# Kernel optimization log

Hardware: AMD Instinct MI355X
Metric: run time of the kernel (lower is better)

The kernel has to match this reference:

```python
import jax, jax.numpy as jnp
import numpy as np

N_NODES = 50000
N_EDGES = 1600000
HID = 128
REST = 96  # (hidden//4) x 1e vectors = 32*3
N_MP = 2


def _linear_init(key, fan_in, fan_out):
    return jax.random.normal(key, (fan_in, fan_out), dtype=jnp.float32) / np.sqrt(fan_in)


def setup_inputs() -> dict:
    key = jax.random.key(0)
    ks = jax.random.split(key, 16)
    h = jax.random.normal(ks[0], (N_NODES, HID + REST), dtype=jnp.float32)
    edge_index = jax.random.randint(ks[1], (2, N_EDGES), 0, N_NODES, dtype=jnp.int32)
    edge_len = jax.random.uniform(ks[2], (N_EDGES,), dtype=jnp.float32) * 5.0
    # ScalarMessagePassing MLPs: Linear(2*HID+1 -> HID), SiLU, Linear(HID -> HID), stacked per layer
    mp_w1 = jnp.stack([_linear_init(ks[3 + i], 2 * HID + 1, HID) for i in range(N_MP)])
    mp_b1 = jnp.zeros((N_MP, HID), dtype=jnp.float32)
    mp_w2 = jnp.stack([_linear_init(ks[5 + i], HID, HID) for i in range(N_MP)])
    mp_b2 = jnp.zeros((N_MP, HID), dtype=jnp.float32)
    # NodeUpdateMLP: Linear(HID -> HID), SiLU, Linear(HID -> HID)
    nu_w1 = _linear_init(ks[7], HID, HID)
    nu_b1 = jnp.zeros((HID,), dtype=jnp.float32)
    nu_w2 = _linear_init(ks[8], HID, HID)
    nu_b2 = jnp.zeros((HID,), dtype=jnp.float32)
    return dict(h=h, edge_index=edge_index, edge_len=edge_len,
                mp_w1=mp_w1, mp_b1=mp_b1, mp_w2=mp_w2, mp_b2=mp_b2,
                nu_w1=nu_w1, nu_b1=nu_b1, nu_w2=nu_w2, nu_b2=nu_b2)


def _scalar_mp(scalars, sender, receiver, edge_len, w1, b1, w2, b2):
    # gather -> MLP -> index_add scatter, residual on scalar channels
    msg_in = jnp.concatenate([scalars[sender], scalars[receiver], edge_len[:, None]], axis=-1)  # [E, 2H+1]
    msgs = jax.nn.silu(msg_in @ w1 + b1) @ w2 + b2  # [E, H]
    agg = jax.ops.segment_sum(msgs, receiver, num_segments=scalars.shape[0])  # [N, H]
    return scalars + agg


def reference(h, edge_index, edge_len, mp_w1, mp_b1, mp_w2, mp_b2, nu_w1, nu_b1, nu_w2, nu_b2):
    scalars, rest = h[..., :HID], h[..., HID:]
    sender, receiver = edge_index[0], edge_index[1]
    for i in range(N_MP):
        scalars = _scalar_mp(scalars, sender, receiver, edge_len,
                             mp_w1[i], mp_b1[i], mp_w2[i], mp_b2[i])
    # NodeUpdateMLP: scalars + MLP(scalars)
    scalars = scalars + (jax.nn.silu(scalars @ nu_w1 + nu_b1) @ nu_w2 + nu_b2)
    return jnp.concatenate([scalars, rest], axis=-1)
```

## Files before the change

kernel.cpp:

```cpp
#include <hip/hip_runtime.h>
#include <hip/hip_fp16.h>


#define NFEAT 224
#define RBITS 8
#define NB 196
#define CAP 10240

typedef _Float16 v8h __attribute__((ext_vector_type(8)));
typedef _Float16 v2h __attribute__((ext_vector_type(2)));
typedef float f32x4 __attribute__((ext_vector_type(4)));

#define MFMA16(a, b, c) __builtin_amdgcn_mfma_f32_16x16x32_f16(a, b, c, 0, 0, 0)

__device__ __forceinline__ float silu_f(float x) {
    float e = __expf(-x);
    return x * __builtin_amdgcn_rcpf(1.0f + e);
}

__global__ void k_prep(const float* __restrict__ mp_w1, const float* __restrict__ mp_w2,
                       const float* __restrict__ nu_w1, const float* __restrict__ nu_w2,
                       _Float16* __restrict__ Wp,
                       const float4* __restrict__ h4, float4* __restrict__ out4, int N) {
    if (blockIdx.x < 8) {
        const float* srcs[8] = {
            mp_w1, mp_w1 + 16384, mp_w2,
            mp_w1 + 32896, mp_w1 + 32896 + 16384, mp_w2 + 16384,
            nu_w1, nu_w2
        };
        const float* W = srcs[blockIdx.x];
        _Float16* dst = Wp + (size_t)blockIdx.x * 16384;
        for (int i = 0; i < 8; ++i) {
            int u = threadIdx.x + i * 256;
            int nt = u >> 8;
            int kt = (u >> 6) & 3;
            int lane = u & 63;
            int kb = kt * 32 + (lane >> 4) * 8;
            int n = nt * 16 + (lane & 15);
#pragma unroll
            for (int j = 0; j < 8; ++j)
                dst[(size_t)u * 8 + j] = (_Float16)W[(size_t)(kb + j) * 128 + n];
        }
    } else {
        int b = blockIdx.x - 8;
        int t = threadIdx.x;
        if (t < 240) {
            int r = b * 10 + t / 24;
            int c = t % 24;
            if (r < N) out4[(size_t)r * 56 + 32 + c] = h4[(size_t)r * 56 + 32 + c];
        }
    }
}

__global__ void cs_bucket(const int* __restrict__ recv, const int* __restrict__ sender,
                          const float* __restrict__ elen, int* __restrict__ cnt,
                          int* __restrict__ br, unsigned* __restrict__ bsl,
                          int E, int chunk) {
    __shared__ int lhist[256];
    __shared__ int lcur[256];
    int t = threadIdx.x;
    int start = blockIdx.x * chunk;
    int end = start + chunk; if (end > E) end = E;
    lhist[t] = 0;
    __syncthreads();
    for (int i = start + t; i < end; i += 256)
        atomicAdd(&lhist[recv[i] >> RBITS], 1);
    __syncthreads();
    if (t < NB) {
        int c = lhist[t];
        lcur[t] = t * CAP + (c ? atomicAdd(&cnt[t], c) : 0);
    }
    __syncthreads();
    for (int i = start + t; i < end; i += 256) {
        int r = recv[i];
        int pos = atomicAdd(&lcur[r >> RBITS], 1);
        br[pos] = r;
        bsl[pos] = (unsigned)sender[i] |
                   ((unsigned)__half_as_ushort(__float2half_rn(elen[i])) << 16);
    }
}

__global__ void cs_csr(const int* __restrict__ cnt, const int* __restrict__ br,
                       const unsigned* __restrict__ bsl,
                       int* __restrict__ deg, int* __restrict__ rowstart,
                       unsigned* __restrict__ epack, int N) {
    __shared__ int hist[256];
    __shared__ int sh[256];
    __shared__ int lcur[256];
    int t = threadIdx.x;
    int b = blockIdx.x;
    int r0 = b << RBITS;
    int e0 = b * CAP;
    int e1 = e0 + cnt[b];
    hist[t] = 0;
    __syncthreads();
    for (int i = e0 + t; i < e1; i += 256)
        atomicAdd(&hist[br[i] & 255], 1);
    __syncthreads();
    sh[t] = hist[t];
    __syncthreads();
    for (int off = 1; off < 256; off <<= 1) {
        int add = (t >= off) ? sh[t - off] : 0;
        __syncthreads();
        sh[t] += add;
        __syncthreads();
    }
    int excl = (t == 0) ? 0 : sh[t - 1];
    lcur[t] = e0 + excl;
    int r = r0 + t;
    if (r < N) { deg[r] = hist[t]; rowstart[r] = e0 + excl; }
    __syncthreads();
    for (int i = e0 + t; i < e1; i += 256) {
        int rr = br[i];
        int pos = atomicAdd(&lcur[rr & 255], 1);
        epack[pos] = bsl[i];
    }
}


#define MM_STAGE_A_F32(Aptr, ldA)                                           \
    _Pragma("unroll") for (int i = 0; i < 4; ++i) {                         \
        int u = threadIdx.x + i * 256;                                      \
        int r = u >> 4;                                                     \
        int g = u & 15;                                                     \
        int gr = blockIdx.x * 64 + r;                                       \
        float4 x0 = make_float4(0.f, 0.f, 0.f, 0.f);                        \
        float4 x1 = x0;                                                     \
        if (gr < M) {                                                       \
            const float* s_ = (Aptr) + (size_t)gr * (ldA) + g * 8;          \
            x0 = *(const float4*)s_;                                        \
            x1 = *(const float4*)(s_ + 4);                                  \
        }                                                                   \
        v8h hv;                                                             \
        hv[0] = (_Float16)x0.x; hv[1] = (_Float16)x0.y;                     \
        hv[2] = (_Float16)x0.z; hv[3] = (_Float16)x0.w;                     \
        hv[4] = (_Float16)x1.x; hv[5] = (_Float16)x1.y;                     \
        hv[6] = (_Float16)x1.z; hv[7] = (_Float16)x1.w;                     \
        Af[((r >> 4) * 4 + (g >> 2)) * 64 + (g & 3) * 16 + (r & 15)] = hv;  \
    }

#define MM_STAGE_A_F16(Aptr)                                                \
    _Pragma("unroll") for (int i = 0; i < 4; ++i) {                         \
        int u = threadIdx.x + i * 256;                                      \
        int r = u >> 4;                                                     \
        int g = u & 15;                                                     \
        int gr = blockIdx.x * 64 + r;                                       \
        float4 x = make_float4(0.f, 0.f, 0.f, 0.f);                         \
        if (gr < M) x = *(const float4*)((Aptr) + (size_t)gr * 128 + g * 8);\
        *(float4*)&Af[((r >> 4) * 4 + (g >> 2)) * 64 + (g & 3) * 16 + (r & 15)] = x; \
    }

#define MM_WAVE_PROLOG                                                      \
    __syncthreads();                                                        \
    const int wv = threadIdx.x >> 6;                                        \
    const int lane = threadIdx.x & 63;                                      \
    const int q_ = lane >> 4;                                               \
    const int c0_ = lane & 15;                                              \
    v8h a0 = Af[(wv * 4 + 0) * 64 + lane];                                  \
    v8h a1 = Af[(wv * 4 + 1) * 64 + lane];                                  \
    v8h a2 = Af[(wv * 4 + 2) * 64 + lane];                                  \
    v8h a3 = Af[(wv * 4 + 3) * 64 + lane];                                  \
    const int grb = blockIdx.x * 64 + wv * 16 + q_ * 4;

#define MM_RELOAD_A(SRC)                                                    \
    a0 = SRC[(wv * 4 + 0) * 64 + lane];                                     \
    a1 = SRC[(wv * 4 + 1) * 64 + lane];                                     \
    a2 = SRC[(wv * 4 + 2) * 64 + lane];                                     \
    a3 = SRC[(wv * 4 + 3) * 64 + lane];

#define MM_COMPUTE_B(WPTR, ...)                                             \
    {                                                                       \
        const v8h* Bp_ = (const v8h*)(WPTR) + lane;                         \
        _Pragma("unroll") for (int nt = 0; nt < 8; ++nt) {                  \
            v8h b0 = Bp_[nt * 256];                                         \
            v8h b1v = Bp_[nt * 256 + 64];                                   \
            v8h b2v = Bp_[nt * 256 + 128];                                  \
            v8h b3v = Bp_[nt * 256 + 192];                                  \
            f32x4 c = {0.f, 0.f, 0.f, 0.f};                                 \
            c = MFMA16(a0, b0, c);                                          \
            c = MFMA16(a1, b1v, c);                                         \
            c = MFMA16(a2, b2v, c);                                         \
            c = MFMA16(a3, b3v, c);                                         \
            const int col = nt * 16 + c0_;                                  \
            __VA_ARGS__                                                     \
        }                                                                   \
    }

#define MM_EXCHANGE_IDX                                                     \
    int kt = col >> 5;                                                      \
    int o = col & 31;                                                       \
    int qp = o >> 3;                                                        \
    int j = o & 7;                                                          \
    int base = ((wv * 4 + kt) * 64 + qp * 16 + q_ * 4) * 8 + j;

__launch_bounds__(256)
__global__ void k_mm_xsrb2(const float* __restrict__ A, int ldA,
                           const _Float16* __restrict__ Wp0, const float* __restrict__ b1,
                           _Float16* __restrict__ Xs, _Float16* __restrict__ Xrb, int M) {
    __shared__ v8h Af[1024];
    MM_STAGE_A_F32(A, ldA)
    MM_WAVE_PROLOG
    MM_COMPUTE_B(Wp0, {
        _Pragma("unroll") for (int i = 0; i < 4; ++i) {
            int gr = grb + i;
            if (gr < M) Xs[(size_t)gr * 128 + col] = (_Float16)c[i];
        }
    })
    MM_COMPUTE_B(Wp0 + 16384, {
        float bc = b1[col];
        _Pragma("unroll") for (int i = 0; i < 4; ++i) {
            int gr = grb + i;
            if (gr < M) Xrb[(size_t)gr * 128 + col] = (_Float16)(c[i] + bc);
        }
    })
}

__launch_bounds__(256)
__global__ void k_mm_accxsrb(const _Float16* __restrict__ P, const _Float16* __restrict__ Ww2,
                             const float* __restrict__ b2, const int* __restrict__ deg,
                             const float* __restrict__ Sin, int ldSin,
                             float* __restrict__ Sout,
                             const _Float16* __restrict__ Wp1, const float* __restrict__ b1,
                             _Float16* __restrict__ Xs, _Float16* __restrict__ Xrb, int M) {
    __shared__ v8h Af[1024];
    __shared__ v8h Af2[1024];
    MM_STAGE_A_F16(P)
    MM_WAVE_PROLOG
    _Float16* A2 = (_Float16*)Af2;
    MM_COMPUTE_B(Ww2, {
        float bc = b2[col];
        MM_EXCHANGE_IDX
        _Pragma("unroll") for (int i = 0; i < 4; ++i) {
            int gr = grb + i;
            float sv = 0.f;
            if (gr < M) {
                sv = Sin[(size_t)gr * ldSin + col] + c[i] + bc * (float)deg[gr];
                Sout[(size_t)gr * 128 + col] = sv;
            }
            A2[base + i * 8] = (_Float16)sv;
        }
    })
    __syncthreads();
    MM_RELOAD_A(Af2)
    MM_COMPUTE_B(Wp1, {
        _Pragma("unroll") for (int i = 0; i < 4; ++i) {
            int gr = grb + i;
            if (gr < M) Xs[(size_t)gr * 128 + col] = (_Float16)c[i];
        }
    })
    MM_COMPUTE_B(Wp1 + 16384, {
        float bc = b1[col];
        _Pragma("unroll") for (int i = 0; i < 4; ++i) {
            int gr = grb + i;
            if (gr < M) Xrb[(size_t)gr * 128 + col] = (_Float16)(c[i] + bc);
        }
    })
}

__launch_bounds__(256)
__global__ void k_mm_accnode(const _Float16* __restrict__ P, const _Float16* __restrict__ Ww2,
                             const float* __restrict__ b2, const int* __restrict__ deg,
                             const float* __restrict__ Sin,
                             const _Float16* __restrict__ Wn1, const float* __restrict__ nb1,
                             const _Float16* __restrict__ Wn2, const float* __restrict__ nb2,
                             float* __restrict__ out, int M) {
    __shared__ v8h Af[1024];
    __shared__ v8h Af2[1024];
    MM_STAGE_A_F16(P)
    MM_WAVE_PROLOG
    float s2v[8][4];
    _Float16* A2 = (_Float16*)Af2;
    MM_COMPUTE_B(Ww2, {
        float bc = b2[col];
        MM_EXCHANGE_IDX
        _Pragma("unroll") for (int i = 0; i < 4; ++i) {
            int gr = grb + i;
            float sv = 0.f;
            if (gr < M) sv = Sin[(size_t)gr * 128 + col] + c[i] + bc * (float)deg[gr];
            s2v[nt][i] = sv;
            A2[base + i * 8] = (_Float16)sv;
        }
    })
    __syncthreads();
    MM_RELOAD_A(Af2)
    _Float16* A3 = (_Float16*)Af;
    MM_COMPUTE_B(Wn1, {
        float bc = nb1[col];
        MM_EXCHANGE_IDX
        _Pragma("unroll") for (int i = 0; i < 4; ++i)
            A3[base + i * 8] = (_Float16)silu_f(c[i] + bc);
    })
    __syncthreads();
    MM_RELOAD_A(Af)
    MM_COMPUTE_B(Wn2, {
        float bc = nb2[col];
        _Pragma("unroll") for (int i = 0; i < 4; ++i) {
            int gr = grb + i;
            if (gr < M)
                out[(size_t)gr * NFEAT + col] = s2v[nt][i] + c[i] + bc;
        }
    })
}

__device__ __forceinline__ v2h silu2_pk(v2h pre) {
    const v2h h27 = {(_Float16)27.f, (_Float16)27.f};
    const v2h hp3 = {(_Float16)3.f, (_Float16)3.f};
    const v2h hn3 = {(_Float16)-3.f, (_Float16)-3.f};
    v2h h = pre * (_Float16)0.5f;
    v2h z = __builtin_elementwise_min(__builtin_elementwise_max(h, hn3), hp3);
    v2h z2 = z * z;
    v2h num = z * (z2 + h27);
    v2h den = z2 * (_Float16)9.f + h27;
    __half2 rd = h2rcp(__builtin_bit_cast(__half2, den));
    v2h u = num * __builtin_bit_cast(v2h, rd);
    return h * u + h;
}

__launch_bounds__(256)
__global__ void k_edge(const v2h* __restrict__ Xs, const v2h* __restrict__ Xrb,
                       const float* __restrict__ w1L, const unsigned* __restrict__ epack,
                       const int* __restrict__ rowstart, const int* __restrict__ deg,
                       v2h* __restrict__ P, int N) {
    int wid = (blockIdx.x * blockDim.x + threadIdx.x) >> 6;
    int lane = threadIdx.x & 63;
    if (wid >= N) return;
    int lo = __builtin_amdgcn_readfirstlane(rowstart[wid]);
    int dg = __builtin_amdgcn_readfirstlane(deg[wid]);
    const unsigned* ep = epack + lo;
    v2h xr = Xrb[(size_t)wid * 64 + lane];
    float2 wlf = *(const float2*)(w1L + lane * 2);
    v2h wl = {(_Float16)wlf.x, (_Float16)wlf.y};
    float ax = 0.f, ay = 0.f;
    int k = 0;
    unsigned pc[8];
    v2h xc[8];
    if (dg >= 8) {
#pragma unroll
        for (int u = 0; u < 8; ++u) pc[u] = ep[u];
#pragma unroll
        for (int u = 0; u < 8; ++u)
            xc[u] = Xs[(size_t)(pc[u] & 0xFFFFu) * 64 + lane];
    }
    for (; k + 16 <= dg; k += 8) {
        unsigned pn[8];
        v2h xn[8];
#pragma unroll
        for (int u = 0; u < 8; ++u) pn[u] = ep[k + 8 + u];
#pragma unroll
        for (int u = 0; u < 8; ++u)
            xn[u] = Xs[(size_t)(pn[u] & 0xFFFFu) * 64 + lane];
        v2h t2 = {(_Float16)0.f, (_Float16)0.f};
#pragma unroll
        for (int u = 0; u < 8; ++u) {
            _Float16 lv = __builtin_bit_cast(_Float16, (unsigned short)(pc[u] >> 16));
            v2h pre = xc[u] + xr + lv * wl;
            t2 = t2 + silu2_pk(pre);
        }
        ax += (float)t2[0]; ay += (float)t2[1];
#pragma unroll
        for (int u = 0; u < 8; ++u) { pc[u] = pn[u]; xc[u] = xn[u]; }
    }
    if (k + 8 <= dg) {
        v2h t2 = {(_Float16)0.f, (_Float16)0.f};
#pragma unroll
        for (int u = 0; u < 8; ++u) {
            _Float16 lv = __builtin_bit_cast(_Float16, (unsigned short)(pc[u] >> 16));
            v2h pre = xc[u] + xr + lv * wl;
            t2 = t2 + silu2_pk(pre);
        }
        ax += (float)t2[0]; ay += (float)t2[1];
        k += 8;
    }
    for (; k < dg; ++k) {
        unsigned p = ep[k];
        _Float16 lv = __builtin_bit_cast(_Float16, (unsigned short)(p >> 16));
        v2h x = Xs[(size_t)(p & 0xFFFFu) * 64 + lane];
        v2h pre = x + xr + lv * wl;
        v2h s = silu2_pk(pre);
        ax += (float)s[0]; ay += (float)s[1];
    }
    v2h o = {(_Float16)ax, (_Float16)ay};
    P[(size_t)wid * 64 + lane] = o;
}

extern "C" void kernel_launch(void* const* d_in, const int* in_sizes, int n_in,
                              void* d_out, int out_size, void* d_ws, size_t ws_size,
                              hipStream_t stream) {
    const float* h      = (const float*)d_in[0];
    const int*   eidx   = (const int*)d_in[1];
    const float* elen   = (const float*)d_in[2];
    const float* mp_w1  = (const float*)d_in[3];
    const float* mp_b1  = (const float*)d_in[4];
    const float* mp_w2  = (const float*)d_in[5];
    const float* mp_b2  = (const float*)d_in[6];
    const float* nu_w1  = (const float*)d_in[7];
    const float* nu_b1  = (const float*)d_in[8];
    const float* nu_w2  = (const float*)d_in[9];
    const float* nu_b2  = (const float*)d_in[10];
    float* out = (float*)d_out;

    const int N = in_sizes[0] / NFEAT;
    const int E = in_sizes[2];
    const int* sender   = eidx;
    const int* receiver = eidx + E;

    char* w = (char*)d_ws;
    auto alloc = [&](size_t bytes) -> char* {
        char* p = w;
        w += (bytes + 255) & ~(size_t)255;
        return p;
    };
    float*    S1    = (float*)alloc((size_t)N * 128 * 4);
    _Float16* Pf    = (_Float16*)alloc((size_t)N * 128 * 2);
    _Float16* Xs16  = (_Float16*)alloc((size_t)N * 128 * 2);
    _Float16* Xrb16 = (_Float16*)alloc((size_t)N * 128 * 2);
    _Float16* Wp    = (_Float16*)alloc((size_t)8 * 16384 * 2);
    int*      br    = (int*)alloc((size_t)NB * CAP * 4);
    unsigned* bsl   = (unsigned*)alloc((size_t)NB * CAP * 4);
    unsigned* epack = (unsigned*)alloc((size_t)NB * CAP * 4);
    int*      deg      = (int*)alloc((size_t)N * 4);
    int*      rowstart = (int*)alloc((size_t)N * 4);
    int*      cnt      = (int*)alloc((size_t)NB * 4);

    (void)hipMemsetAsync(cnt, 0, (size_t)NB * 4, stream);
    k_prep<<<8 + (N + 9) / 10, 256, 0, stream>>>(mp_w1, mp_w2, nu_w1, nu_w2, Wp,
                                                 (const float4*)h, (float4*)out, N);
    const int chunk = 4096;
    cs_bucket<<<(E + chunk - 1) / chunk, 256, 0, stream>>>(receiver, sender, elen, cnt,
                                                           br, bsl, E, chunk);
    cs_csr<<<NB, 256, 0, stream>>>(cnt, br, bsl, deg, rowstart, epack, N);

    const int gb = (N + 63) / 64;
    const int eb = (N * 64 + 255) / 256;

    k_mm_xsrb2<<<gb, 256, 0, stream>>>(h, NFEAT, Wp, mp_b1, Xs16, Xrb16, N);
    k_edge<<<eb, 256, 0, stream>>>((const v2h*)Xs16, (const v2h*)Xrb16,
                                   mp_w1 + 32768, epack, rowstart, deg, (v2h*)Pf, N);
    k_mm_accxsrb<<<gb, 256, 0, stream>>>(Pf, Wp + (size_t)2 * 16384, mp_b2, deg,
                                         h, NFEAT, S1,
                                         Wp + (size_t)3 * 16384, mp_b1 + 128,
                                         Xs16, Xrb16, N);
    k_edge<<<eb, 256, 0, stream>>>((const v2h*)Xs16, (const v2h*)Xrb16,
                                   mp_w1 + 32896 + 32768, epack, rowstart, deg,
                                   (v2h*)Pf, N);
    k_mm_accnode<<<gb, 256, 0, stream>>>(Pf, Wp + (size_t)5 * 16384, mp_b2 + 128, deg,
                                         S1,
                                         Wp + (size_t)6 * 16384, nu_b1,
                                         Wp + (size_t)7 * 16384, nu_b2,
                                         out, N);
}
```

Before: 396.5 us.

## Process two receiver rows per wave with prefetched first blocks and masked tail

Each wavefront in the edge kernel now handles two destination rows instead of one. The first 8-edge block of both rows is loaded up front, so gather latency for the second row overlaps with work on the first. The scalar remainder loop is replaced by a masked 8-wide block that clamps indices and zeroes the unused lanes. This halves the grid, adds register pressure from the two prefetch buffers, and spends some wasted silu work on padded edges.

```diff
diff --git a/kernel.cpp b/kernel.cpp
--- a/kernel.cpp
+++ b/kernel.cpp
@@ -316,6 +316,66 @@
     return h * u + h;
 }
 
+__device__ __forceinline__ void load_blk_pay(const unsigned* __restrict__ ep, int k,
+                                             int last, unsigned p[8]) {
+#pragma unroll
+    for (int u = 0; u < 8; ++u) { int i = k + u; p[u] = ep[i <= last ? i : last]; }
+}
+
+__device__ __forceinline__ void load_blk_x(const v2h* __restrict__ Xs, int lane,
+                                           const unsigned p[8], v2h x[8]) {
+#pragma unroll
+    for (int u = 0; u < 8; ++u) x[u] = Xs[(size_t)(p[u] & 0xFFFFu) * 64 + lane];
+}
+
+__device__ __forceinline__ void blk_full(const unsigned p[8], const v2h x[8],
+                                         v2h xr, v2h wl, float& ax, float& ay) {
+    v2h t2 = {(_Float16)0.f, (_Float16)0.f};
+#pragma unroll
+    for (int u = 0; u < 8; ++u) {
+        _Float16 lv = __builtin_bit_cast(_Float16, (unsigned short)(p[u] >> 16));
+        v2h pre = x[u] + xr + lv * wl;
+        t2 = t2 + silu2_pk(pre);
+    }
+    ax += (float)t2[0]; ay += (float)t2[1];
+}
+
+__device__ __forceinline__ void blk_mask(const unsigned p[8], const v2h x[8],
+                                         v2h xr, v2h wl, int rem, float& ax, float& ay) {
+    v2h t2 = {(_Float16)0.f, (_Float16)0.f};
+#pragma unroll
+    for (int u = 0; u < 8; ++u) {
+        _Float16 lv = __builtin_bit_cast(_Float16, (unsigned short)(p[u] >> 16));
+        v2h pre = x[u] + xr + lv * wl;
+        v2h s = silu2_pk(pre);
+        _Float16 mu = (u < rem) ? (_Float16)1.f : (_Float16)0.f;
+        v2h mv = {mu, mu};
+        t2 = t2 + s * mv;
+    }
+    ax += (float)t2[0]; ay += (float)t2[1];
+}
+
+__device__ __forceinline__ v2h edge_row(const unsigned* __restrict__ ep, int dg,
+                                        v2h xr, v2h wl, const v2h* __restrict__ Xs,
+                                        int lane, unsigned pc[8], v2h xc[8]) {
+    float ax = 0.f, ay = 0.f;
+    int nb = (dg + 7) >> 3;
+    int last = dg - 1;
+    int k = 0;
+    for (int b = 0; b + 1 < nb; ++b, k += 8) {
+        unsigned pn[8];
+        v2h xn[8];
+        load_blk_pay(ep, k + 8, last, pn);
+        load_blk_x(Xs, lane, pn, xn);
+        blk_full(pc, xc, xr, wl, ax, ay);
+#pragma unroll
+        for (int u = 0; u < 8; ++u) { pc[u] = pn[u]; xc[u] = xn[u]; }
+    }
+    blk_mask(pc, xc, xr, wl, dg - k, ax, ay);
+    v2h o = {(_Float16)ax, (_Float16)ay};
+    return o;
+}
+
 __launch_bounds__(256)
 __global__ void k_edge(const v2h* __restrict__ Xs, const v2h* __restrict__ Xrb,
                        const float* __restrict__ w1L, const unsigned* __restrict__ epack,
@@ -323,64 +383,31 @@
                        v2h* __restrict__ P, int N) {
     int wid = (blockIdx.x * blockDim.x + threadIdx.x) >> 6;
     int lane = threadIdx.x & 63;
-    if (wid >= N) return;
-    int lo = __builtin_amdgcn_readfirstlane(rowstart[wid]);
-    int dg = __builtin_amdgcn_readfirstlane(deg[wid]);
-    const unsigned* ep = epack + lo;
-    v2h xr = Xrb[(size_t)wid * 64 + lane];
+    int r0 = wid * 2;
+    if (r0 >= N) return;
+    int r1 = r0 + 1;
+    int dg0 = __builtin_amdgcn_readfirstlane(deg[r0]);
+    int lo0 = __builtin_amdgcn_readfirstlane(rowstart[r0]);
+    int dg1 = 0, lo1 = 0;
+    if (r1 < N) {
+        dg1 = __builtin_amdgcn_readfirstlane(deg[r1]);
+        lo1 = __builtin_amdgcn_readfirstlane(rowstart[r1]);
+    }
     float2 wlf = *(const float2*)(w1L + lane * 2);
     v2h wl = {(_Float16)wlf.x, (_Float16)wlf.y};
-    float ax = 0.f, ay = 0.f;
-    int k = 0;
-    unsigned pc[8];
-    v2h xc[8];
-    if (dg >= 8) {
-#pragma unroll
-        for (int u = 0; u < 8; ++u) pc[u] = ep[u];
-#pragma unroll
-        for (int u = 0; u < 8; ++u)
-            xc[u] = Xs[(size_t)(pc[u] & 0xFFFFu) * 64 + lane];
-    }
-    for (; k + 16 <= dg; k += 8) {
-        unsigned pn[8];
-        v2h xn[8];
-#pragma unroll
-        for (int u = 0; u < 8; ++u) pn[u] = ep[k + 8 + u];
-#pragma unroll
-        for (int u = 0; u < 8; ++u)
-            xn[u] = Xs[(size_t)(pn[u] & 0xFFFFu) * 64 + lane];
-        v2h t2 = {(_Float16)0.f, (_Float16)0.f};
-#pragma unroll
-        for (int u = 0; u < 8; ++u) {
-            _Float16 lv = __builtin_bit_cast(_Float16, (unsigned short)(pc[u] >> 16));
-            v2h pre = xc[u] + xr + lv * wl;
-            t2 = t2 + silu2_pk(pre);
-        }
-        ax += (float)t2[0]; ay += (float)t2[1];
-#pragma unroll
-        for (int u = 0; u < 8; ++u) { pc[u] = pn[u]; xc[u] = xn[u]; }
-    }
-    if (k + 8 <= dg) {
-        v2h t2 = {(_Float16)0.f, (_Float16)0.f};
-#pragma unroll
-        for (int u = 0; u < 8; ++u) {
-            _Float16 lv = __builtin_bit_cast(_Float16, (unsigned short)(pc[u] >> 16));
-            v2h pre = xc[u] + xr + lv * wl;
-            t2 = t2 + silu2_pk(pre);
-        }
-        ax += (float)t2[0]; ay += (float)t2[1];
-        k += 8;
-    }
-    for (; k < dg; ++k) {
-        unsigned p = ep[k];
-        _Float16 lv = __builtin_bit_cast(_Float16, (unsigned short)(p >> 16));
-        v2h x = Xs[(size_t)(p & 0xFFFFu) * 64 + lane];
-        v2h pre = x + xr + lv * wl;
-        v2h s = silu2_pk(pre);
-        ax += (float)s[0]; ay += (float)s[1];
-    }
-    v2h o = {(_Float16)ax, (_Float16)ay};
-    P[(size_t)wid * 64 + lane] = o;
+    const unsigned* ep0 = epack + lo0;
+    const unsigned* ep1 = epack + lo1;
+    unsigned pc0[8]; v2h xc0[8];
+    unsigned pc1[8]; v2h xc1[8];
+    if (dg0) { load_blk_pay(ep0, 0, dg0 - 1, pc0); load_blk_x(Xs, lane, pc0, xc0); }
+    if (dg1) { load_blk_pay(ep1, 0, dg1 - 1, pc1); load_blk_x(Xs, lane, pc1, xc1); }
+    v2h xr0 = Xrb[(size_t)r0 * 64 + lane];
+    v2h zero = {(_Float16)0.f, (_Float16)0.f};
+    v2h xr1 = (r1 < N) ? Xrb[(size_t)r1 * 64 + lane] : zero;
+    v2h o0 = dg0 ? edge_row(ep0, dg0, xr0, wl, Xs, lane, pc0, xc0) : zero;
+    v2h o1 = dg1 ? edge_row(ep1, dg1, xr1, wl, Xs, lane, pc1, xc1) : zero;
+    P[(size_t)r0 * 64 + lane] = o0;
+    if (r1 < N) P[(size_t)r1 * 64 + lane] = o1;
 }
 
 extern "C" void kernel_launch(void* const* d_in, const int* in_sizes, int n_in,
@@ -431,7 +458,7 @@
     cs_csr<<<NB, 256, 0, stream>>>(cnt, br, bsl, deg, rowstart, epack, N);
 
     const int gb = (N + 63) / 64;
-    const int eb = (N * 64 + 255) / 256;
+    const int eb = (((N + 1) / 2) * 64 + 255) / 256;
 
     k_mm_xsrb2<<<gb, 256, 0, stream>>>(h, NFEAT, Wp, mp_b1, Xs16, Xrb16, N);
     k_edge<<<eb, 256, 0, stream>>>((const v2h*)Xs16, (const v2h*)Xrb16,
```

Result: slower. 436.3 us (+10.0%).
